# Kernel optimization log

Hardware: AMD Instinct MI355X
Metric: run time of the kernel (lower is better)

Reference implementation:

```python
import jax, jax.numpy as jnp
import numpy as np

WEIGHT_CE = 1.0
WEIGHT_DICE = 1.0
EPS = 1e-10
SMOOTH = 1e-5


def setup_inputs() -> dict:
    key = jax.random.key(0)
    k1, k2 = jax.random.split(key)
    B, N, H, W, D = 2, 8, 128, 128, 128
    logits = jax.random.normal(k1, (B, N, H, W, D), dtype=jnp.float32)
    pred = jax.nn.softmax(logits, axis=1)  # module expects softmaxed preds
    target = jax.random.randint(k2, (B, 1, H, W, D), 0, N, dtype=jnp.int32)
    return {"pred": pred, "target": target}


def reference(pred, target):
    # pred: (B, N, H, W, D) softmax probs; target: (B, 1, H, W, D) int labels
    B, N = pred.shape[0], pred.shape[1]
    t = target[:, 0]  # (B, H, W, D)

    # --- CE part (faithful to the original's cross-batch one-hot bug) ---
    # loss[b2, hwd] = -sum_b sum_c 1[t[b2,hwd]==c] * log(pred[b,c,hwd]+eps)
    logp_sum = jnp.sum(jnp.log(pred + EPS), axis=0)  # (N, H, W, D)
    gathered = jnp.take_along_axis(
        jnp.broadcast_to(logp_sum[None], (B,) + logp_sum.shape),
        t[:, None], axis=1)[:, 0]  # (B, H, W, D)
    celoss = -jnp.mean(gathered) / B

    # --- MONAI DiceLoss(softmax=False, to_onehot_y=True), defaults ---
    oh = (t[:, None] == jnp.arange(N, dtype=t.dtype)[None, :, None, None, None]).astype(pred.dtype)  # (B,N,H,W,D)
    inter = jnp.sum(oh * pred, axis=(2, 3, 4))   # (B, N)
    ground_o = jnp.sum(oh, axis=(2, 3, 4))       # (B, N)
    pred_o = jnp.sum(pred, axis=(2, 3, 4))       # (B, N)
    dice = jnp.mean(1.0 - (2.0 * inter + SMOOTH) / (ground_o + pred_o + SMOOTH))

    return WEIGHT_CE * celoss + WEIGHT_DICE * dice
```

## Files before the change

kernel.cpp:

```cpp
#include <hip/hip_runtime.h>

#define S_VOX (128*128*128)
#define QV (S_VOX/4)
#define BLOCKS_PER_PLANE 128
#define CHUNK_Q (QV / BLOCKS_PER_PLANE)
#define EPSF 1e-10f
#define SMOOTHF 1e-5f

#define NACC 49

__device__ __forceinline__ float wave_reduce(float v) {
#pragma unroll
    for (int off = 32; off > 0; off >>= 1)
        v += __shfl_down(v, off, 64);
    return v;
}

__global__ __launch_bounds__(256) void dice_main(const float* __restrict__ pred,
                                                 const int* __restrict__ tgt,
                                                 float* __restrict__ ws) {
    const int plane = blockIdx.x >> 7;
    const int chunk = blockIdx.x & 127;
    const int b = plane >> 3;
    const int n = plane & 7;

    const float4* p4 = (const float4*)pred + (size_t)plane * QV + (size_t)chunk * CHUNK_Q;
    const int4*   ta = (const int4*)tgt + (size_t)b * QV        + (size_t)chunk * CHUNK_Q;
    const int4*   tb = (const int4*)tgt + (size_t)(1 - b) * QV  + (size_t)chunk * CHUNK_Q;

    float po = 0.f, inter = 0.f, ce = 0.f;
    int gc = 0;

#pragma unroll 4
    for (int i = threadIdx.x; i < CHUNK_Q; i += 256) {
        const float4 p  = p4[i];
        const int4   t0 = ta[i];
        const int4   t1 = tb[i];
        po += (p.x + p.y) + (p.z + p.w);
#define SLOT(pv, u, v)                                          \
        {                                                       \
            const int m0 = ((u) == n);                          \
            const int m1 = ((v) == n);                          \
            inter += m0 ? (pv) : 0.f;                           \
            gc    += m0;                                        \
            ce    += (float)(m0 + m1) * __logf((pv) + EPSF);    \
        }
        SLOT(p.x, t0.x, t1.x)
        SLOT(p.y, t0.y, t1.y)
        SLOT(p.z, t0.z, t1.z)
        SLOT(p.w, t0.w, t1.w)
#undef SLOT
    }

    __shared__ float red[4][4];
    const int lane = threadIdx.x & 63;
    const int wave = threadIdx.x >> 6;
    float acc[4] = { ce, inter, (float)gc, po };
#pragma unroll
    for (int i = 0; i < 4; i++) {
        float v = wave_reduce(acc[i]);
        if (lane == 0) red[wave][i] = v;
    }
    __syncthreads();
    if (threadIdx.x < 4) {
        const int i = threadIdx.x;
        const float s = red[0][i] + red[1][i] + red[2][i] + red[3][i];
        int dst;
        if (i == 0)      dst = 0;
        else if (i == 1) dst = 1  + plane;
        else if (i == 2) dst = 17 + plane;
        else             dst = 33 + plane;
        atomicAdd(&ws[dst], s);
    }
}

__global__ void dice_finalize(const float* __restrict__ ws, float* __restrict__ out) {
    const int i = threadIdx.x;
    float term = 0.f;
    if (i < 16) {
        float inter = ws[1 + i];
        float g     = ws[17 + i];
        float p     = ws[33 + i];
        term = 1.0f - (2.0f * inter + SMOOTHF) / (g + p + SMOOTHF);
    }
    term = wave_reduce(term);
    if (i == 0) {
        float celoss = -ws[0] / (4.0f * (float)S_VOX);
        out[0] = celoss + term * (1.0f / 16.0f);
    }
}

extern "C" void kernel_launch(void* const* d_in, const int* in_sizes, int n_in,
                              void* d_out, int out_size, void* d_ws, size_t ws_size,
                              hipStream_t stream) {
    const float* pred = (const float*)d_in[0];
    const int*   tgt  = (const int*)d_in[1];
    float* ws  = (float*)d_ws;
    float* out = (float*)d_out;

    hipMemsetAsync(ws, 0, NACC * sizeof(float), stream);
    dice_main<<<16 * BLOCKS_PER_PLANE, 256, 0, stream>>>(pred, tgt, ws);
    dice_finalize<<<1, 64, 0, stream>>>(ws, out);
}
```

Baseline: 230.6 us.

## Process four class-batch planes per block to cut redundant target reads and logs

Each block now handles two classes for both batches at the same spatial chunk, so the two target tensors are loaded once per four prediction planes instead of once per plane. This cuts target traffic from 32 reads of each label tensor to 4. The CE log terms for the two batches are merged into a single __logf of a product, halving transcendental count. All loads are issued up front for memory-level parallelism, with launch bounds raised to 3 blocks per SIMD. The cost is higher register pressure and more atomics per block, and the log-of-product could underflow for tiny probabilities.

```diff
diff --git a/kernel.cpp b/kernel.cpp
--- a/kernel.cpp
+++ b/kernel.cpp
@@ -2,8 +2,8 @@
 
 #define S_VOX (128*128*128)
 #define QV (S_VOX/4)
-#define BLOCKS_PER_PLANE 128
-#define CHUNK_Q (QV / BLOCKS_PER_PLANE)
+#define CHUNKS 512
+#define CHUNK_Q (QV / CHUNKS)
 #define EPSF 1e-10f
 #define SMOOTHF 1e-5f
 
@@ -16,60 +16,97 @@
     return v;
 }
 
-__global__ __launch_bounds__(256) void dice_main(const float* __restrict__ pred,
-                                                 const int* __restrict__ tgt,
-                                                 float* __restrict__ ws) {
-    const int plane = blockIdx.x >> 7;
-    const int chunk = blockIdx.x & 127;
-    const int b = plane >> 3;
-    const int n = plane & 7;
+__global__ __launch_bounds__(256, 3) void dice_main(const float* __restrict__ pred,
+                                                    const int* __restrict__ tgt,
+                                                    float* __restrict__ ws) {
+    const int chunk = blockIdx.x >> 2;
+    const int j     = blockIdx.x & 3;
+    const int n0 = 2 * j;
 
-    const float4* p4 = (const float4*)pred + (size_t)plane * QV + (size_t)chunk * CHUNK_Q;
-    const int4*   ta = (const int4*)tgt + (size_t)b * QV        + (size_t)chunk * CHUNK_Q;
-    const int4*   tb = (const int4*)tgt + (size_t)(1 - b) * QV  + (size_t)chunk * CHUNK_Q;
+    const size_t cb = (size_t)chunk * CHUNK_Q;
+    const float4* p00 = (const float4*)pred + (size_t)(n0     ) * QV + cb;
+    const float4* p01 = (const float4*)pred + (size_t)(n0 +  1) * QV + cb;
+    const float4* p10 = (const float4*)pred + (size_t)(n0 +  8) * QV + cb;
+    const float4* p11 = (const float4*)pred + (size_t)(n0 +  9) * QV + cb;
+    const int4*   t0p = (const int4*)tgt + cb;
+    const int4*   t1p = (const int4*)tgt + (size_t)QV + cb;
 
-    float po = 0.f, inter = 0.f, ce = 0.f;
-    int gc = 0;
+    float ce = 0.f;
+    float inter[4] = {0.f,0.f,0.f,0.f};
+    float po[4]    = {0.f,0.f,0.f,0.f};
+    int   gc[4]    = {0,0,0,0};
 
-#pragma unroll 4
-    for (int i = threadIdx.x; i < CHUNK_Q; i += 256) {
-        const float4 p  = p4[i];
-        const int4   t0 = ta[i];
-        const int4   t1 = tb[i];
-        po += (p.x + p.y) + (p.z + p.w);
-#define SLOT(pv, u, v)                                          \
-        {                                                       \
-            const int m0 = ((u) == n);                          \
-            const int m1 = ((v) == n);                          \
-            inter += m0 ? (pv) : 0.f;                           \
-            gc    += m0;                                        \
-            ce    += (float)(m0 + m1) * __logf((pv) + EPSF);    \
-        }
-        SLOT(p.x, t0.x, t1.x)
-        SLOT(p.y, t0.y, t1.y)
-        SLOT(p.z, t0.z, t1.z)
-        SLOT(p.w, t0.w, t1.w)
-#undef SLOT
+    const int i0 = threadIdx.x;
+
+    float4 A0[4], A1[4], A2[4], A3[4];
+    int4   TA[4], TB[4];
+#pragma unroll
+    for (int k = 0; k < 4; k++) {
+        const int i = i0 + k * 256;
+        A0[k] = p00[i];
+        A1[k] = p01[i];
+        A2[k] = p10[i];
+        A3[k] = p11[i];
+        TA[k] = t0p[i];
+        TB[k] = t1p[i];
     }
 
-    __shared__ float red[4][4];
+#pragma unroll
+    for (int k = 0; k < 4; k++) {
+        const int4 ta = TA[k], tb = TB[k];
+        const float4 q0 = A0[k], q1 = A1[k], q2 = A2[k], q3 = A3[k];
+
+#define VOXEL(pa, pb, pc, pd, u, v)                                     \
+        {                                                               \
+            const int ua = ((u) == n0);                                 \
+            const int ub = ((u) == n0 + 1);                             \
+            const int va = ((v) == n0);                                 \
+            const int vb = ((v) == n0 + 1);                             \
+            inter[0] += ua ? (pa) : 0.f;  gc[0] += ua;                  \
+            inter[1] += ub ? (pb) : 0.f;  gc[1] += ub;                  \
+            inter[2] += va ? (pc) : 0.f;  gc[2] += va;                  \
+            inter[3] += vb ? (pd) : 0.f;  gc[3] += vb;                  \
+            ce += (float)(ua + va) * __logf(((pa) + EPSF) * ((pc) + EPSF)); \
+            ce += (float)(ub + vb) * __logf(((pb) + EPSF) * ((pd) + EPSF)); \
+            po[0] += (pa); po[1] += (pb); po[2] += (pc); po[3] += (pd); \
+        }
+        VOXEL(q0.x, q1.x, q2.x, q3.x, ta.x, tb.x)
+        VOXEL(q0.y, q1.y, q2.y, q3.y, ta.y, tb.y)
+        VOXEL(q0.z, q1.z, q2.z, q3.z, ta.z, tb.z)
+        VOXEL(q0.w, q1.w, q2.w, q3.w, ta.w, tb.w)
+#undef VOXEL
+    }
+
+    __shared__ float red[4][13];
     const int lane = threadIdx.x & 63;
     const int wave = threadIdx.x >> 6;
-    float acc[4] = { ce, inter, (float)gc, po };
+    float acc[13];
+    acc[0] = ce;
 #pragma unroll
-    for (int i = 0; i < 4; i++) {
+    for (int l = 0; l < 4; l++) {
+        acc[1 + l] = inter[l];
+        acc[5 + l] = (float)gc[l];
+        acc[9 + l] = po[l];
+    }
+#pragma unroll
+    for (int i = 0; i < 13; i++) {
         float v = wave_reduce(acc[i]);
         if (lane == 0) red[wave][i] = v;
     }
     __syncthreads();
-    if (threadIdx.x < 4) {
+    if (threadIdx.x < 13) {
         const int i = threadIdx.x;
         const float s = red[0][i] + red[1][i] + red[2][i] + red[3][i];
         int dst;
-        if (i == 0)      dst = 0;
-        else if (i == 1) dst = 1  + plane;
-        else if (i == 2) dst = 17 + plane;
-        else             dst = 33 + plane;
+        if (i == 0) {
+            dst = 0;
+        } else {
+            const int l = (i - 1) & 3;
+            const int plane = ((l >> 1) * 8) + n0 + (l & 1);
+            if (i <= 4)      dst = 1  + plane;
+            else if (i <= 8) dst = 17 + plane;
+            else             dst = 33 + plane;
+        }
         atomicAdd(&ws[dst], s);
     }
 }
@@ -99,6 +136,6 @@
     float* out = (float*)d_out;
 
     hipMemsetAsync(ws, 0, NACC * sizeof(float), stream);
-    dice_main<<<16 * BLOCKS_PER_PLANE, 256, 0, stream>>>(pred, tgt, ws);
+    dice_main<<<CHUNKS * 4, 256, 0, stream>>>(pred, tgt, ws);
     dice_finalize<<<1, 64, 0, stream>>>(ws, out);
 }
```

After: 230.3 us. About the same (-0.1%).

## Pack targets into byte codes and process both batches per block with pipelined loads

Applied to the files above, without the earlier changes.

Adds a pre-pass that packs the two batches' integer labels into one byte per voxel, so the main kernel reads 1 byte of label data per voxel instead of 8. Each block now covers the same class in both batches and combines the two log terms into one log of a product. Loads are manually software-pipelined with sched barriers, and the atomic accumulators are replicated per XCD to reduce contention. The cost is an extra kernel launch and a small encoding pass, plus a slight numerical change from taking the log of a product.

```diff
diff --git a/kernel.cpp b/kernel.cpp
--- a/kernel.cpp
+++ b/kernel.cpp
@@ -2,12 +2,14 @@
 
 #define S_VOX (128*128*128)
 #define QV (S_VOX/4)
-#define BLOCKS_PER_PLANE 128
-#define CHUNK_Q (QV / BLOCKS_PER_PLANE)
+#define SEGS 256
+#define SEG_Q (QV / SEGS)
 #define EPSF 1e-10f
 #define SMOOTHF 1e-5f
 
-#define NACC 49
+#define NREP 8
+#define REP_STRIDE 64
+#define CODES_OFF 4096
 
 __device__ __forceinline__ float wave_reduce(float v) {
 #pragma unroll
@@ -16,61 +18,92 @@
     return v;
 }
 
+__global__ __launch_bounds__(256) void encode_tgt(const int* __restrict__ tgt,
+                                                  unsigned char* __restrict__ codes) {
+    const int idx = blockIdx.x * 256 + threadIdx.x;
+    const int4 a = ((const int4*)tgt)[idx];
+    const int4 b = ((const int4*)tgt)[QV + idx];
+    uchar4 c;
+    c.x = (unsigned char)(a.x | (b.x << 3));
+    c.y = (unsigned char)(a.y | (b.y << 3));
+    c.z = (unsigned char)(a.z | (b.z << 3));
+    c.w = (unsigned char)(a.w | (b.w << 3));
+    ((uchar4*)codes)[idx] = c;
+}
+
 __global__ __launch_bounds__(256) void dice_main(const float* __restrict__ pred,
-                                                 const int* __restrict__ tgt,
+                                                 const unsigned char* __restrict__ codes,
                                                  float* __restrict__ ws) {
-    const int plane = blockIdx.x >> 7;
-    const int chunk = blockIdx.x & 127;
-    const int b = plane >> 3;
-    const int n = plane & 7;
+    const int xcd   = blockIdx.x & 7;
+    const int r     = blockIdx.x >> 3;
+    const int n     = r & 7;
+    const int seg   = ((r >> 3) << 3) | xcd;
 
-    const float4* p4 = (const float4*)pred + (size_t)plane * QV + (size_t)chunk * CHUNK_Q;
-    const int4*   ta = (const int4*)tgt + (size_t)b * QV        + (size_t)chunk * CHUNK_Q;
-    const int4*   tb = (const int4*)tgt + (size_t)(1 - b) * QV  + (size_t)chunk * CHUNK_Q;
+    const size_t base = (size_t)seg * SEG_Q;
+    const float4* p0 = (const float4*)pred + (size_t)n       * QV + base;
+    const float4* p1 = (const float4*)pred + (size_t)(8 + n) * QV + base;
+    const uchar4* cd = (const uchar4*)codes + base;
 
-    float po = 0.f, inter = 0.f, ce = 0.f;
-    int gc = 0;
+    float ce = 0.f, in0 = 0.f, in1 = 0.f, po0 = 0.f, po1 = 0.f;
+    int   g0 = 0, g1 = 0;
 
-#pragma unroll 4
-    for (int i = threadIdx.x; i < CHUNK_Q; i += 256) {
-        const float4 p  = p4[i];
-        const int4   t0 = ta[i];
-        const int4   t1 = tb[i];
-        po += (p.x + p.y) + (p.z + p.w);
-#define SLOT(pv, u, v)                                          \
-        {                                                       \
-            const int m0 = ((u) == n);                          \
-            const int m1 = ((v) == n);                          \
-            inter += m0 ? (pv) : 0.f;                           \
-            gc    += m0;                                        \
-            ce    += (float)(m0 + m1) * __logf((pv) + EPSF);    \
-        }
-        SLOT(p.x, t0.x, t1.x)
-        SLOT(p.y, t0.y, t1.y)
-        SLOT(p.z, t0.z, t1.z)
-        SLOT(p.w, t0.w, t1.w)
-#undef SLOT
+    const int i0 = threadIdx.x;
+
+#define LD(q0_, q1_, c_, k)                                             \
+    { q0_ = p0[i0 + (k) * 256]; q1_ = p1[i0 + (k) * 256]; c_ = cd[i0 + (k) * 256]; }
+
+#define VOX(pa, pb, cc)                                                 \
+    {                                                                   \
+        const int m0 = (((cc) & 7) == n);                               \
+        const int m1 = ((((cc) >> 3) & 7) == n);                        \
+        in0 += m0 ? (pa) : 0.f;  g0 += m0;                              \
+        in1 += m1 ? (pb) : 0.f;  g1 += m1;                              \
+        ce  += (float)(m0 + m1) * __logf(((pa) + EPSF) * ((pb) + EPSF)); \
+        po0 += (pa);  po1 += (pb);                                      \
     }
+#define CONS(q0_, q1_, c_)                                              \
+    {                                                                   \
+        VOX(q0_.x, q1_.x, c_.x)                                         \
+        VOX(q0_.y, q1_.y, c_.y)                                         \
+        VOX(q0_.z, q1_.z, c_.z)                                         \
+        VOX(q0_.w, q1_.w, c_.w)                                         \
+    }
+#define SB __builtin_amdgcn_sched_barrier(0)
 
-    __shared__ float red[4][4];
+    float4 a0, a1, b0, b1, c0, c1;
+    uchar4 ac, bc, cc;
+    LD(a0, a1, ac, 0)
+    LD(b0, b1, bc, 1)
+    SB;
+    LD(c0, c1, cc, 2) SB; CONS(a0, a1, ac)
+    LD(a0, a1, ac, 3) SB; CONS(b0, b1, bc)
+    LD(b0, b1, bc, 4) SB; CONS(c0, c1, cc)
+    LD(c0, c1, cc, 5) SB; CONS(a0, a1, ac)
+    LD(a0, a1, ac, 6) SB; CONS(b0, b1, bc)
+    LD(b0, b1, bc, 7) SB; CONS(c0, c1, cc)
+    CONS(a0, a1, ac)
+    CONS(b0, b1, bc)
+#undef SB
+#undef CONS
+#undef VOX
+#undef LD
+
+    __shared__ float red[4][7];
     const int lane = threadIdx.x & 63;
     const int wave = threadIdx.x >> 6;
-    float acc[4] = { ce, inter, (float)gc, po };
+    float acc[7] = { ce, in0, in1, (float)g0, (float)g1, po0, po1 };
 #pragma unroll
-    for (int i = 0; i < 4; i++) {
-        float v = wave_reduce(acc[i]);
-        if (lane == 0) red[wave][i] = v;
+    for (int k = 0; k < 7; k++) {
+        float v = wave_reduce(acc[k]);
+        if (lane == 0) red[wave][k] = v;
     }
     __syncthreads();
-    if (threadIdx.x < 4) {
-        const int i = threadIdx.x;
-        const float s = red[0][i] + red[1][i] + red[2][i] + red[3][i];
-        int dst;
-        if (i == 0)      dst = 0;
-        else if (i == 1) dst = 1  + plane;
-        else if (i == 2) dst = 17 + plane;
-        else             dst = 33 + plane;
-        atomicAdd(&ws[dst], s);
+    if (threadIdx.x < 7) {
+        const int k = threadIdx.x;
+        const float s = red[0][k] + red[1][k] + red[2][k] + red[3][k];
+        static const int off[7] = { 0, 1, 9, 17, 25, 33, 41 };
+        const int dst = (k == 0) ? 0 : off[k] + n;
+        atomicAdd(&ws[xcd * REP_STRIDE + dst], s);
     }
 }
 
@@ -78,14 +111,21 @@
     const int i = threadIdx.x;
     float term = 0.f;
     if (i < 16) {
-        float inter = ws[1 + i];
-        float g     = ws[17 + i];
-        float p     = ws[33 + i];
+        float inter = 0.f, g = 0.f, p = 0.f;
+#pragma unroll
+        for (int rp = 0; rp < NREP; rp++) {
+            inter += ws[rp * REP_STRIDE + 1  + i];
+            g     += ws[rp * REP_STRIDE + 17 + i];
+            p     += ws[rp * REP_STRIDE + 33 + i];
+        }
         term = 1.0f - (2.0f * inter + SMOOTHF) / (g + p + SMOOTHF);
     }
     term = wave_reduce(term);
     if (i == 0) {
-        float celoss = -ws[0] / (4.0f * (float)S_VOX);
+        float ce = 0.f;
+#pragma unroll
+        for (int rp = 0; rp < NREP; rp++) ce += ws[rp * REP_STRIDE];
+        float celoss = -ce / (4.0f * (float)S_VOX);
         out[0] = celoss + term * (1.0f / 16.0f);
     }
 }
@@ -97,8 +137,10 @@
     const int*   tgt  = (const int*)d_in[1];
     float* ws  = (float*)d_ws;
     float* out = (float*)d_out;
+    unsigned char* codes = (unsigned char*)(ws + CODES_OFF);
 
-    hipMemsetAsync(ws, 0, NACC * sizeof(float), stream);
-    dice_main<<<16 * BLOCKS_PER_PLANE, 256, 0, stream>>>(pred, tgt, ws);
+    hipMemsetAsync(ws, 0, NREP * REP_STRIDE * sizeof(float), stream);
+    encode_tgt<<<QV / 256, 256, 0, stream>>>(tgt, codes);
+    dice_main<<<8 * SEGS, 256, 0, stream>>>(pred, codes, ws);
     dice_finalize<<<1, 64, 0, stream>>>(ws, out);
 }
```

Measured after the change: 216.5 us. -6.1%, faster.
